# Kernel tuning notes

Measured on AMD Instinct MI355X. Metric: run time of the kernel, lower is better.

Reference implementation:

```python
import jax, jax.numpy as jnp
import numpy as np
from jax import lax

B, N, D, H, K = 8, 1024, 384, 6, 7
HD = D // H
EPS = 1e-5


def layer_norm(x, g, b):
    m = jnp.mean(x, axis=-1, keepdims=True)
    v = jnp.mean(jnp.square(x - m), axis=-1, keepdims=True)
    return (x - m) * lax.rsqrt(v + EPS) * g + b


def setup_inputs() -> dict:
    key = jax.random.key(0)
    ks = jax.random.split(key, 12)
    s = 0.02
    return {
        "x": jax.random.normal(ks[0], (B, N, D), jnp.float32),
        "qkv_w": jax.random.normal(ks[1], (3 * D, D), jnp.float32) * s,
        "qkv_b": jnp.zeros((3 * D,), jnp.float32),
        "proj_w": jax.random.normal(ks[2], (D, D), jnp.float32) * s,
        "proj_b": jnp.zeros((D,), jnp.float32),
        "t_before": jnp.eye(H, dtype=jnp.float32) + jax.random.normal(ks[3], (H, H), jnp.float32) * 0.01,
        "t_after": jnp.eye(H, dtype=jnp.float32) + jax.random.normal(ks[4], (H, H), jnp.float32) * 0.01,
        "dw_w": jax.random.normal(ks[5], (D, 1, K), jnp.float32) * s,
        "dw_b": jnp.zeros((D,), jnp.float32),
        "mlp_ln_g": jnp.ones((D,), jnp.float32),
        "mlp_ln_b": jnp.zeros((D,), jnp.float32),
        "norm1_g": jnp.ones((D,), jnp.float32),
        "norm1_b": jnp.zeros((D,), jnp.float32),
        "norm2_g": jnp.ones((D,), jnp.float32),
        "norm2_b": jnp.zeros((D,), jnp.float32),
        "fc1_w": jax.random.normal(ks[6], (4 * D, D), jnp.float32) * s,
        "fc1_b": jnp.zeros((4 * D,), jnp.float32),
        "fc2_w": jax.random.normal(ks[7], (D, 4 * D), jnp.float32) * s,
        "fc2_b": jnp.zeros((D,), jnp.float32),
    }


def reference(x, qkv_w, qkv_b, proj_w, proj_b, t_before, t_after, dw_w, dw_b,
              mlp_ln_g, mlp_ln_b, norm1_g, norm1_b, norm2_g, norm2_b,
              fc1_w, fc1_b, fc2_w, fc2_b):
    # ---- attention branch ----
    h = layer_norm(x, norm1_g, norm1_b)
    qkv = h @ qkv_w.T + qkv_b                                  # (B,N,3D)
    qkv = qkv.reshape(B, N, 3, H, HD).transpose(2, 0, 3, 1, 4)  # (3,B,H,N,hd)
    q, k, v = qkv[0], qkv[1], qkv[2]
    scale = HD ** -0.5
    scores = jnp.einsum('bhnd,bhmd->bhnm', q, k) * scale        # (B,H,N,N)
    scores = jnp.einsum('gh,bhnm->bgnm', t_before, scores)       # head-mix pre-softmax
    probs = jax.nn.softmax(scores, axis=-1)
    probs = jnp.einsum('gh,bhnm->bgnm', t_after, probs)          # head-mix post-softmax
    attn_out = jnp.einsum('bhnm,bhmd->bhnd', probs, v)           # (B,H,N,hd)
    attn_out = attn_out.transpose(0, 2, 1, 3).reshape(B, N, D)
    attn_out = attn_out @ proj_w.T + proj_b
    x = x + attn_out
    # ---- MLP branch ----
    h = layer_norm(x, norm2_g, norm2_b)
    # depthwise conv1d over tokens: (B,D,N), groups=D, same padding
    h_t = h.transpose(0, 2, 1)
    h_t = lax.conv_general_dilated(h_t, dw_w, window_strides=(1,),
                                   padding=[(K // 2, K // 2)],
                                   dimension_numbers=('NCH', 'OIH', 'NCH'),
                                   feature_group_count=D)
    h = h_t.transpose(0, 2, 1) + dw_b
    h = layer_norm(h, mlp_ln_g, mlp_ln_b)
    h = jax.nn.gelu(h @ fc1_w.T + fc1_b, approximate=False)
    h = h @ fc2_w.T + fc2_b
    return x + h
```

## Files before the change

### kernel.cpp

```cpp
#include <hip/hip_runtime.h>
#include <hip/hip_bf16.h>

#define BB 8
#define NN 1024
#define DD 384
#define HH 6
#define HD 64
#define BN 8192
#define D3 1152
#define D4 1536
#define SEC 3145728

typedef __attribute__((ext_vector_type(8))) short short8;
typedef __attribute__((ext_vector_type(4))) float f32x4;
typedef __attribute__((ext_vector_type(2))) float f32x2;

typedef __attribute__((address_space(3))) unsigned char as3_byte;
typedef __attribute__((address_space(1))) const unsigned char as1_byte;

__device__ __forceinline__ void gload16(const void* g, void* l){
  __builtin_amdgcn_global_load_lds((as1_byte*)g, (as3_byte*)l, 16, 0, 0);
}

__device__ __forceinline__ float b2f(unsigned short u){
  union{unsigned int i; float f;} x; x.i=((unsigned int)u)<<16; return x.f;
}
__device__ __forceinline__ unsigned short f2b(float f){
  unsigned int u=__float_as_uint(f);
  return (unsigned short)((u + 0x7FFFu + ((u>>16)&1u))>>16);
}

__global__ void cvt_kernel(const float* __restrict__ w0, const float* __restrict__ w1,
                           const float* __restrict__ w2, const float* __restrict__ w3,
                           unsigned short* __restrict__ out, float* __restrict__ lbuf){
  int i = blockIdx.x*256 + threadIdx.x;
  if (i < 442368)        out[i] = f2b(w0[i]);
  else if (i < 589824)   out[i] = f2b(w1[i - 442368]);
  else if (i < 1179648)  out[i] = f2b(w2[i - 589824]);
  else if (i < 1769472)  out[i] = f2b(w3[i - 1179648]);
  else if (i < 1818624)  lbuf[i - 1769472] = 0.f;
}

template<int OUTBF>
__global__ __launch_bounds__(128)
void ln_kernel(const float* __restrict__ in, const float* __restrict__ gg, const float* __restrict__ bb,
               float* __restrict__ outf, unsigned short* __restrict__ outb){
  int row = blockIdx.x, t = threadIdx.x;
  const float* r = in + (size_t)row*DD;
  float v0=r[t], v1=r[t+128], v2=r[t+256];
  float s=v0+v1+v2, q=v0*v0+v1*v1+v2*v2;
  #pragma unroll
  for (int o=32;o>0;o>>=1){ s+=__shfl_down(s,o); q+=__shfl_down(q,o); }
  __shared__ float ls[2], lq[2];
  if ((t&63)==0){ ls[t>>6]=s; lq[t>>6]=q; }
  __syncthreads();
  float S=ls[0]+ls[1], Q=lq[0]+lq[1];
  float mean=S*(1.0f/DD);
  float rstd=rsqrtf(Q*(1.0f/DD)-mean*mean+1e-5f);
  float o0=(v0-mean)*rstd*gg[t]+bb[t];
  float o1=(v1-mean)*rstd*gg[t+128]+bb[t+128];
  float o2=(v2-mean)*rstd*gg[t+256]+bb[t+256];
  if (OUTBF){ unsigned short* o=outb+(size_t)row*DD; o[t]=f2b(o0); o[t+128]=f2b(o1); o[t+256]=f2b(o2); }
  else      { float* o=outf+(size_t)row*DD; o[t]=o0; o[t+128]=o1; o[t+256]=o2; }
}

__global__ __launch_bounds__(128)
void conv_ln_kernel(const float* __restrict__ h2, const float* __restrict__ dww, const float* __restrict__ dwb,
                    const float* __restrict__ gg, const float* __restrict__ bb, unsigned short* __restrict__ out){
  int row=blockIdx.x, t=threadIdx.x;
  int bi=row>>10, n=row&1023;
  const float* base = h2 + (size_t)(bi<<10)*DD;
  float a[3];
  #pragma unroll
  for (int j=0;j<3;j++){
    int d=t+j*128;
    float acc=dwb[d];
    #pragma unroll
    for (int k=0;k<7;k++){
      int nn=n+k-3;
      if (nn>=0 && nn<NN) acc += dww[d*7+k]*base[(size_t)nn*DD + d];
    }
    a[j]=acc;
  }
  float s=a[0]+a[1]+a[2], q=a[0]*a[0]+a[1]*a[1]+a[2]*a[2];
  #pragma unroll
  for (int o=32;o>0;o>>=1){ s+=__shfl_down(s,o); q+=__shfl_down(q,o); }
  __shared__ float ls[2], lq[2];
  if ((t&63)==0){ ls[t>>6]=s; lq[t>>6]=q; }
  __syncthreads();
  float S=ls[0]+ls[1], Q=lq[0]+lq[1];
  float mean=S*(1.0f/DD);
  float rstd=rsqrtf(Q*(1.0f/DD)-mean*mean+1e-5f);
  unsigned short* o = out + (size_t)row*DD;
  #pragma unroll
  for (int j=0;j<3;j++){
    int d=t+j*128;
    o[d]=f2b((a[j]-mean)*rstd*gg[d]+bb[d]);
  }
}

template<int MODE, int TN>
__global__ __launch_bounds__(256)
void gemm_kernel(const unsigned short* __restrict__ A, const unsigned short* __restrict__ W,
                 const float* __restrict__ bias, const float* __restrict__ resid,
                 float* __restrict__ outf, unsigned short* __restrict__ outb,
                 unsigned char* __restrict__ v8out,
                 int Kdim, int Ncols){
  constexpr int JF = TN/32;
  __shared__ __align__(16) unsigned short lds_a[2][128*32];
  __shared__ __align__(16) unsigned short lds_b[2][TN*32];
  int t=threadIdx.x, lane=t&63, w=t>>6;
  int bm = blockIdx.x*128;
  int bn = blockIdx.y*TN;
  int wr = w>>1, wc = w&1;
  int rm = lane&15, r16 = lane>>4;
  f32x4 acc[4][JF] = {};
  char* ldsa_c = (char*)lds_a;
  char* ldsb_c = (char*)lds_b;
  int abyte[4], bbyte[JF];
  #pragma unroll
  for (int i=0;i<4;i++){
    int ra = wr*64 + i*16 + rm;
    abyte[i] = ra*64 + ((r16 ^ ((ra>>1)&3))*16);
  }
  #pragma unroll
  for (int j=0;j<JF;j++){
    int rb = wc*(TN/2) + j*16 + rm;
    bbyte[j] = rb*64 + ((r16 ^ ((rb>>1)&3))*16);
  }
  auto stage = [&](int buf, int k0){
    #pragma unroll
    for (int c=0;c<2;c++){
      int u = t + c*256;
      int row = u>>2, sl = (u&3) ^ ((row>>1)&3);
      gload16(A + (size_t)(bm+row)*Kdim + k0 + sl*8, ldsa_c + buf*8192 + u*16);
    }
    #pragma unroll
    for (int c=0;c<TN/64;c++){
      int u = t + c*256;
      int row = u>>2, sl = (u&3) ^ ((row>>1)&3);
      gload16(W + (size_t)(bn+row)*Kdim + k0 + sl*8, ldsb_c + buf*(TN*64) + u*16);
    }
  };
  int niter = Kdim>>5;
  stage(0, 0);
  __syncthreads();
  for (int it=0; it<niter; ++it){
    if (it+1<niter) stage((it+1)&1, (it+1)<<5);
    int ab = (it&1)*8192, bb2 = (it&1)*(TN*64);
    short8 af[4], bf[JF];
    #pragma unroll
    for (int i=0;i<4;i++) af[i]=*reinterpret_cast<const short8*>(ldsa_c + ab + abyte[i]);
    #pragma unroll
    for (int j=0;j<JF;j++) bf[j]=*reinterpret_cast<const short8*>(ldsb_c + bb2 + bbyte[j]);
    #pragma unroll
    for (int i=0;i<4;i++)
      #pragma unroll
      for (int j=0;j<JF;j++)
        acc[i][j]=__builtin_amdgcn_mfma_f32_16x16x32_bf16(af[i],bf[j],acc[i][j],0,0,0);
    __syncthreads();
  }
  #pragma unroll
  for (int i=0;i<4;i++){
    #pragma unroll
    for (int j=0;j<JF;j++){
      #pragma unroll
      for (int r=0;r<4;r++){
        int row = bm + wr*64 + i*16 + r16*4 + r;
        int col = bn + wc*(TN/2) + j*16 + rm;
        float v = acc[i][j][r] + bias[col];
        if (MODE==0){
          int c = col/384; int rem = col - c*384; int hh = rem>>6, d = rem&63;
          int bi = row>>10, nn = row&1023;
          if (c==2){
            int pk = __builtin_amdgcn_cvt_pk_fp8_f32(v, v, 0, false);
            v8out[(((size_t)(bi*6+hh))<<16) + ((size_t)d<<10) + nn] = (unsigned char)(pk & 0xff);
          } else {
            if (c==0) v *= 0.125f;
            outb[(size_t)c*SEC + (((size_t)(bi*6+hh))<<16) + (nn<<6) + d] = f2b(v);
          }
        } else if (MODE==1){
          size_t idx = (size_t)row*Ncols + col;
          outf[idx] = resid[idx] + v;
        } else {
          float ge = 0.5f*v*(1.0f+erff(v*0.70710678118654752f));
          outb[(size_t)row*Ncols + col] = f2b(ge);
        }
      }
    }
  }
}

__global__ __launch_bounds__(256, 2)
void smx_kernel(const unsigned short* __restrict__ qkv, const float* __restrict__ tbm,
                unsigned char* __restrict__ E, float* __restrict__ lbuf){
  __shared__ __align__(16) unsigned short Qs[6*16*64];
  __shared__ __align__(16) unsigned short Ks[6*64*64];
  __shared__ float lred[4][6][16];
  int t=threadIdx.x, lane=t&63, w=t>>6;
  int blk = blockIdx.x;
  int b = blk&7, nt = (blk>>3)&63, mh = blk>>9;
  int n0 = nt*16, mbase = mh<<9;
  int c16 = lane&15, r16 = lane>>4;
  const unsigned short* kbase = qkv + SEC + (((size_t)(b*6))<<16);
  #pragma unroll
  for (int i=0;i<3;i++){
    int u = t + i*256;
    int r = u>>3, s = (u&7) ^ (r&7);
    int h = r>>4, n = r&15;
    gload16(qkv + (((size_t)(b*6+h))<<16) + ((size_t)(n0+n)<<6) + s*8,
            (char*)Qs + u*16);
  }
  auto stageK = [&](int m0){
    #pragma unroll
    for (int i=0;i<12;i++){
      int u = t + i*256;
      int r = u>>3, s = (u&7) ^ (r&7);
      int h = r>>6, m = r&63;
      gload16(kbase + (((size_t)h)<<16) + ((size_t)(m0+m)<<6) + s*8,
              (char*)Ks + u*16);
    }
  };
  stageK(mbase);
  float tbr[36];
  #pragma unroll
  for (int i=0;i<36;i++) tbr[i]=tbm[i]*1.44269504088896f;
  __syncthreads();
  int sw = c16&7;
  short8 qf[6][2];
  #pragma unroll
  for (int h=0;h<6;h++){
    int qb = (h*16 + c16)*128;
    qf[h][0] = *(const short8*)((char*)Qs + qb + ((r16^sw)<<4));
    qf[h][1] = *(const short8*)((char*)Qs + qb + (((4+r16)^sw)<<4));
  }
  int kb0 = (w*16 + c16)*128 + ((r16^sw)<<4);
  int kb1 = (w*16 + c16)*128 + (((4+r16)^sw)<<4);
  float lsum[6] = {0.f,0.f,0.f,0.f,0.f,0.f};
  for (int mt=0; mt<8; ++mt){
    int m0 = mbase + mt*64;
    f32x4 aq[6] = {};
    __builtin_amdgcn_s_setprio(1);
    #pragma unroll
    for (int h=0;h<6;h++){
      short8 kf0 = *(const short8*)((char*)Ks + h*8192 + kb0);
      short8 kf1 = *(const short8*)((char*)Ks + h*8192 + kb1);
      aq[h] = __builtin_amdgcn_mfma_f32_16x16x32_bf16(kf0, qf[h][0], aq[h], 0,0,0);
      aq[h] = __builtin_amdgcn_mfma_f32_16x16x32_bf16(kf1, qf[h][1], aq[h], 0,0,0);
    }
    __builtin_amdgcn_s_setprio(0);
    __syncthreads();
    if (mt<7) stageK(m0+64);
    float ef[6][4];
    #pragma unroll
    for (int r=0;r<4;r++){
      float s0=aq[0][r], s1=aq[1][r], s2=aq[2][r],
            s3=aq[3][r], s4=aq[4][r], s5=aq[5][r];
      #pragma unroll
      for (int g=0;g<6;g++){
        float sm = tbr[g*6]*s0 + tbr[g*6+1]*s1 + tbr[g*6+2]*s2
                 + tbr[g*6+3]*s3 + tbr[g*6+4]*s4 + tbr[g*6+5]*s5;
        float e = __builtin_amdgcn_exp2f(sm);
        ef[g][r] = e;
        lsum[g] += e;
      }
    }
    #pragma unroll
    for (int g=0;g<6;g++){
      int pkv = __builtin_amdgcn_cvt_pk_fp8_f32(ef[g][0], ef[g][1], 0, false);
      pkv = __builtin_amdgcn_cvt_pk_fp8_f32(ef[g][2], ef[g][3], pkv, true);
      *(unsigned int*)(E + (((size_t)(b*6+g))<<20) + ((size_t)(n0+c16)<<10) + m0 + w*16 + r16*4)
        = (unsigned int)pkv;
    }
    if (mt<7) __syncthreads();
  }
  #pragma unroll
  for (int g=0;g<6;g++){
    lsum[g] += __shfl_xor(lsum[g],16);
    lsum[g] += __shfl_xor(lsum[g],32);
  }
  if (r16==0){
    #pragma unroll
    for (int g=0;g<6;g++) lred[w][g][c16] = lsum[g];
  }
  __syncthreads();
  if (w==0 && r16==0){
    #pragma unroll
    for (int g=0;g<6;g++){
      float l = lred[0][g][c16]+lred[1][g][c16]+lred[2][g][c16]+lred[3][g][c16];
      atomicAdd(&lbuf[(((size_t)(b*6+g))<<10) + n0 + c16], l);
    }
  }
}

__global__ __launch_bounds__(256, 2)
void pvmix_kernel(const unsigned char* __restrict__ E, const unsigned char* __restrict__ V8,
                  const float* __restrict__ lbuf, const float* __restrict__ tam,
                  unsigned short* __restrict__ outp){
  __shared__ __align__(16) unsigned char Es[6*16*64];
  __shared__ __align__(16) unsigned char Vs[6*64*64];
  __shared__ __align__(16) unsigned char pms[6*16*64];
  int t=threadIdx.x, lane=t&63, w=t>>6;
  int b = blockIdx.x&7, nt = blockIdx.x>>3;
  int n0 = nt*16;
  int c16 = lane&15, r16 = lane>>4;
  int mn = t&15, mg = (t>>4)&7, gh = t>>7;
  float cf[3][6];
  #pragma unroll
  for (int g=0;g<6;g++){
    float iv = 256.0f/lbuf[(((size_t)(b*6+g))<<10) + n0 + mn];
    #pragma unroll
    for (int j=0;j<3;j++) cf[j][g] = tam[(gh*3+j)*6 + g]*iv;
  }
  auto stageE = [&](int m0){
    #pragma unroll
    for (int i=0;i<2;i++){
      int u = t + i*256;
      if (u<384){
        int r = u>>2, s = (u&3) ^ (r&3);
        int g = r>>4, n = r&15;
        gload16(E + (((size_t)(b*6+g))<<20) + ((size_t)(n0+n)<<10) + m0 + s*16,
                (char*)Es + u*16);
      }
    }
  };
  auto stageV = [&](int m0){
    #pragma unroll
    for (int i=0;i<6;i++){
      int u = t + i*256;
      int r = u>>2, s = (u&3) ^ (r&3);
      int g = r>>6, d = r&63;
      gload16(V8 + (((size_t)(b*6+g))<<16) + ((size_t)d<<10) + m0 + s*16,
              (char*)Vs + u*16);
    }
  };
  stageE(0); stageV(0);
  __syncthreads();
  f32x4 acc[6] = {};
  for (int mt=0; mt<16; ++mt){
    float e[6][8];
    #pragma unroll
    for (int g=0;g<6;g++){
      int row = g*16 + mn;
      int byteo = row*64 + ((mg*8) ^ ((row&3)<<4));
      unsigned int lo = *(const unsigned int*)(Es + byteo);
      unsigned int hi = *(const unsigned int*)(Es + byteo + 4);
      f32x2 p0 = __builtin_amdgcn_cvt_pk_f32_fp8(lo, false);
      f32x2 p1 = __builtin_amdgcn_cvt_pk_f32_fp8(lo, true);
      f32x2 p2 = __builtin_amdgcn_cvt_pk_f32_fp8(hi, false);
      f32x2 p3 = __builtin_amdgcn_cvt_pk_f32_fp8(hi, true);
      e[g][0]=p0.x; e[g][1]=p0.y; e[g][2]=p1.x; e[g][3]=p1.y;
      e[g][4]=p2.x; e[g][5]=p2.y; e[g][6]=p3.x; e[g][7]=p3.y;
    }
    #pragma unroll
    for (int j=0;j<3;j++){
      float pm[8];
      #pragma unroll
      for (int m=0;m<8;m++)
        pm[m] = cf[j][0]*e[0][m]+cf[j][1]*e[1][m]+cf[j][2]*e[2][m]
              + cf[j][3]*e[3][m]+cf[j][4]*e[4][m]+cf[j][5]*e[5][m];
      int d0 = __builtin_amdgcn_cvt_pk_fp8_f32(pm[0], pm[1], 0, false);
      d0 = __builtin_amdgcn_cvt_pk_fp8_f32(pm[2], pm[3], d0, true);
      int d1 = __builtin_amdgcn_cvt_pk_fp8_f32(pm[4], pm[5], 0, false);
      d1 = __builtin_amdgcn_cvt_pk_fp8_f32(pm[6], pm[7], d1, true);
      int prow = (gh*3+j)*16 + mn;
      int pbyte = prow*64 + ((mg*8) ^ ((mn&7)<<3));
      *(unsigned int*)(pms + pbyte)     = (unsigned int)d0;
      *(unsigned int*)(pms + pbyte + 4) = (unsigned int)d1;
    }
    __syncthreads();
    if (mt<15) stageE((mt+1)*64);
    #pragma unroll
    for (int g=0;g<6;g++){
      int arow = g*16 + c16;
      int vrow = g*64 + w*16 + c16;
      #pragma unroll
      for (int kk=0;kk<2;kk++){
        long af = *(const long*)(pms + arow*64 + ((kk*32 + r16*8) ^ ((c16&7)<<3)));
        long bf = *(const long*)(Vs + vrow*64
                   + ((((kk*2 + (r16>>1)) ^ (vrow&3))<<4) + ((r16&1)<<3)));
        acc[g] = __builtin_amdgcn_mfma_f32_16x16x32_fp8_fp8(af, bf, acc[g], 0,0,0);
      }
    }
    __syncthreads();
    if (mt<15) stageV((mt+1)*64);
  }
  #pragma unroll
  for (int g=0;g<6;g++)
    #pragma unroll
    for (int r=0;r<4;r++){
      int n = n0 + r16*4 + r;
      int d = g*64 + w*16 + c16;
      outp[((size_t)(b*1024 + n))*DD + d] = f2b(acc[g][r] * 0.00390625f);
    }
}

extern "C" void kernel_launch(void* const* d_in, const int* in_sizes, int n_in,
                              void* d_out, int out_size, void* d_ws, size_t ws_size,
                              hipStream_t stream){
  const float* x      = (const float*)d_in[0];
  const float* qkv_w  = (const float*)d_in[1];
  const float* qkv_b  = (const float*)d_in[2];
  const float* proj_w = (const float*)d_in[3];
  const float* proj_b = (const float*)d_in[4];
  const float* t_before=(const float*)d_in[5];
  const float* t_after =(const float*)d_in[6];
  const float* dw_w   = (const float*)d_in[7];
  const float* dw_b   = (const float*)d_in[8];
  const float* mlp_g  = (const float*)d_in[9];
  const float* mlp_b  = (const float*)d_in[10];
  const float* n1_g   = (const float*)d_in[11];
  const float* n1_b   = (const float*)d_in[12];
  const float* n2_g   = (const float*)d_in[13];
  const float* n2_b   = (const float*)d_in[14];
  const float* fc1_w  = (const float*)d_in[15];
  const float* fc1_b  = (const float*)d_in[16];
  const float* fc2_w  = (const float*)d_in[17];
  const float* fc2_b  = (const float*)d_in[18];
  float* out = (float*)d_out;
  char* ws = (char*)d_ws;
  unsigned short* qkvwb = (unsigned short*)(ws + 0);
  unsigned short* projwb= (unsigned short*)(ws + 884736);
  unsigned short* fc1wb = (unsigned short*)(ws + 1179648);
  unsigned short* fc2wb = (unsigned short*)(ws + 2359296);
  unsigned short* hb    = (unsigned short*)(ws + 3538944);
  unsigned short* qkvb  = (unsigned short*)(ws + 9830400);
  unsigned char*  V8    = (unsigned char*) (ws + 28704768);
  float*          lbuf  = (float*)        (ws + 31850496);
  unsigned char*  Ebuf  = (unsigned char*) (ws + 34996224);
  unsigned short* attnb = (unsigned short*)(ws + 85327872);
  float*          x2    = (float*)(ws + 91619328);
  float* h2 = (float*)qkvb;
  unsigned short* hcln = hb;
  unsigned short* fc1o = (unsigned short*)Ebuf;

  cvt_kernel<<<7104,256,0,stream>>>(qkv_w, proj_w, fc1_w, fc2_w, qkvwb, lbuf);

  ln_kernel<1><<<BN,128,0,stream>>>(x, n1_g, n1_b, nullptr, hb);
  { dim3 g(BN/128, D3/128); gemm_kernel<0,128><<<g,256,0,stream>>>(hb, qkvwb, qkv_b, nullptr, nullptr, qkvb, V8, DD, D3); }
  smx_kernel<<<1024,256,0,stream>>>(qkvb, t_before, Ebuf, lbuf);
  pvmix_kernel<<<512,256,0,stream>>>(Ebuf, V8, lbuf, t_after, attnb);
  { dim3 g(BN/128, DD/64); gemm_kernel<1,64><<<g,256,0,stream>>>(attnb, projwb, proj_b, x, x2, nullptr, nullptr, DD, DD); }
  ln_kernel<0><<<BN,128,0,stream>>>(x2, n2_g, n2_b, h2, nullptr);
  conv_ln_kernel<<<BN,128,0,stream>>>(h2, dw_w, dw_b, mlp_g, mlp_b, hcln);
  { dim3 g(BN/128, D4/128); gemm_kernel<2,128><<<g,256,0,stream>>>(hcln, fc1wb, fc1_b, nullptr, nullptr, fc1o, nullptr, DD, D4); }
  { dim3 g(BN/128, DD/64); gemm_kernel<1,64><<<g,256,0,stream>>>(fc1o, fc2wb, fc2_b, x2, out, nullptr, nullptr, D4, DD); }
}
```

Before: 208.0 us.

## Store Q/K as FP8 and use FP8 MFMA with 32-row query tiles in softmax

The QKV GEMM now writes Q and K as FP8 bytes instead of bf16, and folds the attention scale into the head-mix coefficients rather than scaling Q. The scores kernel loads these FP8 tiles with an adjusted swizzle and uses fp8 MFMA instructions. Each block now handles 32 query rows, which halves the grid and doubles the reuse of every staged K tile. The aim is to halve Q/K memory traffic and LDS footprint and to raise MFMA throughput, at the cost of lower precision in the attention scores.

```diff
diff --git a/kernel.cpp b/kernel.cpp
--- a/kernel.cpp
+++ b/kernel.cpp
@@ -104,7 +104,7 @@
 void gemm_kernel(const unsigned short* __restrict__ A, const unsigned short* __restrict__ W,
                  const float* __restrict__ bias, const float* __restrict__ resid,
                  float* __restrict__ outf, unsigned short* __restrict__ outb,
-                 unsigned char* __restrict__ v8out,
+                 unsigned char* __restrict__ qk8out, unsigned char* __restrict__ v8out,
                  int Kdim, int Ncols){
   constexpr int JF = TN/32;
   __shared__ __align__(16) unsigned short lds_a[2][128*32];
@@ -172,12 +172,11 @@
         if (MODE==0){
           int c = col/384; int rem = col - c*384; int hh = rem>>6, d = rem&63;
           int bi = row>>10, nn = row&1023;
+          unsigned char pk = (unsigned char)(__builtin_amdgcn_cvt_pk_fp8_f32(v, v, 0, false) & 0xff);
           if (c==2){
-            int pk = __builtin_amdgcn_cvt_pk_fp8_f32(v, v, 0, false);
-            v8out[(((size_t)(bi*6+hh))<<16) + ((size_t)d<<10) + nn] = (unsigned char)(pk & 0xff);
+            v8out[(((size_t)(bi*6+hh))<<16) + ((size_t)d<<10) + nn] = pk;
           } else {
-            if (c==0) v *= 0.125f;
-            outb[(size_t)c*SEC + (((size_t)(bi*6+hh))<<16) + (nn<<6) + d] = f2b(v);
+            qk8out[(size_t)c*SEC + (((size_t)(bi*6+hh))<<16) + ((size_t)nn<<6) + d] = pk;
           }
         } else if (MODE==1){
           size_t idx = (size_t)row*Ncols + col;
@@ -191,105 +190,108 @@
   }
 }
 
-__global__ __launch_bounds__(256, 2)
-void smx_kernel(const unsigned short* __restrict__ qkv, const float* __restrict__ tbm,
+__global__ __launch_bounds__(256, 4)
+void smx_kernel(const unsigned char* __restrict__ qk8, const float* __restrict__ tbm,
                 unsigned char* __restrict__ E, float* __restrict__ lbuf){
-  __shared__ __align__(16) unsigned short Qs[6*16*64];
-  __shared__ __align__(16) unsigned short Ks[6*64*64];
-  __shared__ float lred[4][6][16];
+  __shared__ __align__(16) unsigned char Qs[6*32*64];
+  __shared__ __align__(16) unsigned char Ks[6*64*64];
+  __shared__ float lred[4][6][32];
   int t=threadIdx.x, lane=t&63, w=t>>6;
   int blk = blockIdx.x;
-  int b = blk&7, nt = (blk>>3)&63, mh = blk>>9;
-  int n0 = nt*16, mbase = mh<<9;
+  int b = blk&7, nt = (blk>>3)&31, mh = blk>>8;
+  int n0 = nt*32, mbase = mh<<9;
   int c16 = lane&15, r16 = lane>>4;
-  const unsigned short* kbase = qkv + SEC + (((size_t)(b*6))<<16);
+  int mq = w*16;
+  const unsigned char* q8 = qk8;
+  const unsigned char* k8 = qk8 + SEC;
   #pragma unroll
   for (int i=0;i<3;i++){
     int u = t + i*256;
-    int r = u>>3, s = (u&7) ^ (r&7);
-    int h = r>>4, n = r&15;
-    gload16(qkv + (((size_t)(b*6+h))<<16) + ((size_t)(n0+n)<<6) + s*8,
-            (char*)Qs + u*16);
+    int r = u>>2, s = (u&3) ^ (r&3);
+    int h = r>>5, n = r&31;
+    gload16(q8 + (((size_t)(b*6+h))<<16) + ((size_t)(n0+n)<<6) + s*16, (char*)Qs + u*16);
   }
   auto stageK = [&](int m0){
     #pragma unroll
-    for (int i=0;i<12;i++){
+    for (int i=0;i<6;i++){
       int u = t + i*256;
-      int r = u>>3, s = (u&7) ^ (r&7);
+      int r = u>>2, s = (u&3) ^ (r&3);
       int h = r>>6, m = r&63;
-      gload16(kbase + (((size_t)h)<<16) + ((size_t)(m0+m)<<6) + s*8,
-              (char*)Ks + u*16);
+      gload16(k8 + (((size_t)(b*6+h))<<16) + ((size_t)(m0+m)<<6) + s*16, (char*)Ks + u*16);
     }
   };
   stageK(mbase);
   float tbr[36];
   #pragma unroll
-  for (int i=0;i<36;i++) tbr[i]=tbm[i]*1.44269504088896f;
-  __syncthreads();
-  int sw = c16&7;
-  short8 qf[6][2];
-  #pragma unroll
-  for (int h=0;h<6;h++){
-    int qb = (h*16 + c16)*128;
-    qf[h][0] = *(const short8*)((char*)Qs + qb + ((r16^sw)<<4));
-    qf[h][1] = *(const short8*)((char*)Qs + qb + (((4+r16)^sw)<<4));
-  }
-  int kb0 = (w*16 + c16)*128 + ((r16^sw)<<4);
-  int kb1 = (w*16 + c16)*128 + (((4+r16)^sw)<<4);
-  float lsum[6] = {0.f,0.f,0.f,0.f,0.f,0.f};
+  for (int i=0;i<36;i++) tbr[i] = tbm[i]*0.125f*1.44269504088896f;
+  __syncthreads();
+  float lsum[6][2] = {};
   for (int mt=0; mt<8; ++mt){
     int m0 = mbase + mt*64;
-    f32x4 aq[6] = {};
+    f32x4 aq[6][2] = {};
     __builtin_amdgcn_s_setprio(1);
     #pragma unroll
     for (int h=0;h<6;h++){
-      short8 kf0 = *(const short8*)((char*)Ks + h*8192 + kb0);
-      short8 kf1 = *(const short8*)((char*)Ks + h*8192 + kb1);
-      aq[h] = __builtin_amdgcn_mfma_f32_16x16x32_bf16(kf0, qf[h][0], aq[h], 0,0,0);
-      aq[h] = __builtin_amdgcn_mfma_f32_16x16x32_bf16(kf1, qf[h][1], aq[h], 0,0,0);
+      int krow = h*64 + mq + c16;
+      #pragma unroll
+      for (int kk=0;kk<2;kk++){
+        long kf = *(const long*)(Ks + krow*64 + (((kk*2+(r16>>1)) ^ (krow&3))<<4) + ((r16&1)<<3));
+        #pragma unroll
+        for (int ih=0;ih<2;ih++){
+          int qrow = h*32 + ih*16 + c16;
+          long qf = *(const long*)(Qs + qrow*64 + (((kk*2+(r16>>1)) ^ (qrow&3))<<4) + ((r16&1)<<3));
+          aq[h][ih] = __builtin_amdgcn_mfma_f32_16x16x32_fp8_fp8(kf, qf, aq[h][ih], 0,0,0);
+        }
+      }
     }
     __builtin_amdgcn_s_setprio(0);
     __syncthreads();
     if (mt<7) stageK(m0+64);
-    float ef[6][4];
-    #pragma unroll
-    for (int r=0;r<4;r++){
-      float s0=aq[0][r], s1=aq[1][r], s2=aq[2][r],
-            s3=aq[3][r], s4=aq[4][r], s5=aq[5][r];
+    #pragma unroll
+    for (int ih=0;ih<2;ih++){
+      float ef[6][4];
+      #pragma unroll
+      for (int r=0;r<4;r++){
+        float s0=aq[0][ih][r], s1=aq[1][ih][r], s2=aq[2][ih][r],
+              s3=aq[3][ih][r], s4=aq[4][ih][r], s5=aq[5][ih][r];
+        #pragma unroll
+        for (int g=0;g<6;g++){
+          float sm = tbr[g*6]*s0 + tbr[g*6+1]*s1 + tbr[g*6+2]*s2
+                   + tbr[g*6+3]*s3 + tbr[g*6+4]*s4 + tbr[g*6+5]*s5;
+          float e = __builtin_amdgcn_exp2f(sm);
+          ef[g][r] = e;
+          lsum[g][ih] += e;
+        }
+      }
       #pragma unroll
       for (int g=0;g<6;g++){
-        float sm = tbr[g*6]*s0 + tbr[g*6+1]*s1 + tbr[g*6+2]*s2
-                 + tbr[g*6+3]*s3 + tbr[g*6+4]*s4 + tbr[g*6+5]*s5;
-        float e = __builtin_amdgcn_exp2f(sm);
-        ef[g][r] = e;
-        lsum[g] += e;
-      }
-    }
+        int pkv = __builtin_amdgcn_cvt_pk_fp8_f32(ef[g][0], ef[g][1], 0, false);
+        pkv = __builtin_amdgcn_cvt_pk_fp8_f32(ef[g][2], ef[g][3], pkv, true);
+        *(unsigned int*)(E + (((size_t)(b*6+g))<<20) + ((size_t)(n0+ih*16+c16)<<10) + m0 + mq + r16*4)
+          = (unsigned int)pkv;
+      }
+    }
+    if (mt<7) __syncthreads();
+  }
+  #pragma unroll
+  for (int g=0;g<6;g++)
+    #pragma unroll
+    for (int ih=0;ih<2;ih++){
+      lsum[g][ih] += __shfl_xor(lsum[g][ih],16);
+      lsum[g][ih] += __shfl_xor(lsum[g][ih],32);
+    }
+  if (r16==0){
     #pragma unroll
     for (int g=0;g<6;g++){
-      int pkv = __builtin_amdgcn_cvt_pk_fp8_f32(ef[g][0], ef[g][1], 0, false);
-      pkv = __builtin_amdgcn_cvt_pk_fp8_f32(ef[g][2], ef[g][3], pkv, true);
-      *(unsigned int*)(E + (((size_t)(b*6+g))<<20) + ((size_t)(n0+c16)<<10) + m0 + w*16 + r16*4)
-        = (unsigned int)pkv;
-    }
-    if (mt<7) __syncthreads();
-  }
-  #pragma unroll
-  for (int g=0;g<6;g++){
-    lsum[g] += __shfl_xor(lsum[g],16);
-    lsum[g] += __shfl_xor(lsum[g],32);
-  }
-  if (r16==0){
-    #pragma unroll
-    for (int g=0;g<6;g++) lred[w][g][c16] = lsum[g];
-  }
-  __syncthreads();
-  if (w==0 && r16==0){
-    #pragma unroll
-    for (int g=0;g<6;g++){
-      float l = lred[0][g][c16]+lred[1][g][c16]+lred[2][g][c16]+lred[3][g][c16];
-      atomicAdd(&lbuf[(((size_t)(b*6+g))<<10) + n0 + c16], l);
-    }
+      lred[w][g][c16]    = lsum[g][0];
+      lred[w][g][16+c16] = lsum[g][1];
+    }
+  }
+  __syncthreads();
+  if (t<192){
+    int g = t>>5, n32 = t&31;
+    float l = lred[0][g][n32]+lred[1][g][n32]+lred[2][g][n32]+lred[3][g][n32];
+    atomicAdd(&lbuf[(((size_t)(b*6+g))<<10) + n0 + n32], l);
   }
 }
 
@@ -424,25 +426,25 @@
   unsigned short* fc1wb = (unsigned short*)(ws + 1179648);
   unsigned short* fc2wb = (unsigned short*)(ws + 2359296);
   unsigned short* hb    = (unsigned short*)(ws + 3538944);
-  unsigned short* qkvb  = (unsigned short*)(ws + 9830400);
+  unsigned char*  qk8   = (unsigned char*) (ws + 9830400);
   unsigned char*  V8    = (unsigned char*) (ws + 28704768);
   float*          lbuf  = (float*)        (ws + 31850496);
   unsigned char*  Ebuf  = (unsigned char*) (ws + 34996224);
   unsigned short* attnb = (unsigned short*)(ws + 85327872);
   float*          x2    = (float*)(ws + 91619328);
-  float* h2 = (float*)qkvb;
+  float* h2 = (float*)qk8;
   unsigned short* hcln = hb;
   unsigned short* fc1o = (unsigned short*)Ebuf;
 
   cvt_kernel<<<7104,256,0,stream>>>(qkv_w, proj_w, fc1_w, fc2_w, qkvwb, lbuf);
 
   ln_kernel<1><<<BN,128,0,stream>>>(x, n1_g, n1_b, nullptr, hb);
-  { dim3 g(BN/128, D3/128); gemm_kernel<0,128><<<g,256,0,stream>>>(hb, qkvwb, qkv_b, nullptr, nullptr, qkvb, V8, DD, D3); }
-  smx_kernel<<<1024,256,0,stream>>>(qkvb, t_before, Ebuf, lbuf);
+  { dim3 g(BN/128, D3/128); gemm_kernel<0,128><<<g,256,0,stream>>>(hb, qkvwb, qkv_b, nullptr, nullptr, nullptr, qk8, V8, DD, D3); }
+  smx_kernel<<<512,256,0,stream>>>(qk8, t_before, Ebuf, lbuf);
   pvmix_kernel<<<512,256,0,stream>>>(Ebuf, V8, lbuf, t_after, attnb);
-  { dim3 g(BN/128, DD/64); gemm_kernel<1,64><<<g,256,0,stream>>>(attnb, projwb, proj_b, x, x2, nullptr, nullptr, DD, DD); }
+  { dim3 g(BN/128, DD/64); gemm_kernel<1,64><<<g,256,0,stream>>>(attnb, projwb, proj_b, x, x2, nullptr, nullptr, nullptr, DD, DD); }
   ln_kernel<0><<<BN,128,0,stream>>>(x2, n2_g, n2_b, h2, nullptr);
   conv_ln_kernel<<<BN,128,0,stream>>>(h2, dw_w, dw_b, mlp_g, mlp_b, hcln);
-  { dim3 g(BN/128, D4/128); gemm_kernel<2,128><<<g,256,0,stream>>>(hcln, fc1wb, fc1_b, nullptr, nullptr, fc1o, nullptr, DD, D4); }
-  { dim3 g(BN/128, DD/64); gemm_kernel<1,64><<<g,256,0,stream>>>(fc1o, fc2wb, fc2_b, x2, out, nullptr, nullptr, D4, DD); }
-}
+  { dim3 g(BN/128, D4/128); gemm_kernel<2,128><<<g,256,0,stream>>>(hcln, fc1wb, fc1_b, nullptr, nullptr, fc1o, nullptr, nullptr, DD, D4); }
+  { dim3 g(BN/128, DD/64); gemm_kernel<1,64><<<g,256,0,stream>>>(fc1o, fc2wb, fc2_b, x2, out, nullptr, nullptr, nullptr, D4, DD); }
+}
```

Measured after the change: 241.8 us. +16.2%, slower.

## Store Q/K as fp8 in MFMA fragment layout and drop LDS staging in softmax

Applied to the files above, without the earlier changes.

The QKV GEMM now writes Q and K as fp8 in a pre-swizzled fragment layout, so the softmax kernel loads MFMA operands straight from global memory and uses fp8 MFMA instead of staging bf16 tiles through LDS with barriers. The 1/8 scale moves into the head-mix matrix. The row-sum atomics are replaced with per-half partial sums that pvmix adds together, which also removes the zeroing in the conversion kernel. Occupancy hint raised to 4. Risk: lower Q/K precision in the scores and uncoalesced byte-wide scattered stores from the GEMM epilogue.

```diff
diff --git a/kernel.cpp b/kernel.cpp
--- a/kernel.cpp
+++ b/kernel.cpp
@@ -14,6 +14,7 @@
 typedef __attribute__((ext_vector_type(8))) short short8;
 typedef __attribute__((ext_vector_type(4))) float f32x4;
 typedef __attribute__((ext_vector_type(2))) float f32x2;
+typedef long v2i64 __attribute__((ext_vector_type(2)));
 
 typedef __attribute__((address_space(3))) unsigned char as3_byte;
 typedef __attribute__((address_space(1))) const unsigned char as1_byte;
@@ -32,13 +33,12 @@
 
 __global__ void cvt_kernel(const float* __restrict__ w0, const float* __restrict__ w1,
                            const float* __restrict__ w2, const float* __restrict__ w3,
-                           unsigned short* __restrict__ out, float* __restrict__ lbuf){
+                           unsigned short* __restrict__ out){
   int i = blockIdx.x*256 + threadIdx.x;
   if (i < 442368)        out[i] = f2b(w0[i]);
   else if (i < 589824)   out[i] = f2b(w1[i - 442368]);
   else if (i < 1179648)  out[i] = f2b(w2[i - 589824]);
   else if (i < 1769472)  out[i] = f2b(w3[i - 1179648]);
-  else if (i < 1818624)  lbuf[i - 1769472] = 0.f;
 }
 
 template<int OUTBF>
@@ -104,7 +104,7 @@
 void gemm_kernel(const unsigned short* __restrict__ A, const unsigned short* __restrict__ W,
                  const float* __restrict__ bias, const float* __restrict__ resid,
                  float* __restrict__ outf, unsigned short* __restrict__ outb,
-                 unsigned char* __restrict__ v8out,
+                 unsigned char* __restrict__ qk8out, unsigned char* __restrict__ v8out,
                  int Kdim, int Ncols){
   constexpr int JF = TN/32;
   __shared__ __align__(16) unsigned short lds_a[2][128*32];
@@ -172,12 +172,14 @@
         if (MODE==0){
           int c = col/384; int rem = col - c*384; int hh = rem>>6, d = rem&63;
           int bi = row>>10, nn = row&1023;
+          unsigned char pk = (unsigned char)(__builtin_amdgcn_cvt_pk_fp8_f32(v, v, 0, false) & 0xff);
           if (c==2){
-            int pk = __builtin_amdgcn_cvt_pk_fp8_f32(v, v, 0, false);
-            v8out[(((size_t)(bi*6+hh))<<16) + ((size_t)d<<10) + nn] = (unsigned char)(pk & 0xff);
+            v8out[(((size_t)(bi*6+hh))<<16) + ((size_t)d<<10) + nn] = pk;
           } else {
-            if (c==0) v *= 0.125f;
-            outb[(size_t)c*SEC + (((size_t)(bi*6+hh))<<16) + (nn<<6) + d] = f2b(v);
+            size_t fa = ((size_t)c*SEC)
+                      + ((((size_t)(bi*6+hh))<<6) + (nn>>4))*1024
+                      + ((((d>>3)&3)*16 + (nn&15))<<4) + ((d>>5)*8) + (d&7);
+            qk8out[fa] = pk;
           }
         } else if (MODE==1){
           size_t idx = (size_t)row*Ncols + col;
@@ -191,66 +193,37 @@
   }
 }
 
-__global__ __launch_bounds__(256, 2)
-void smx_kernel(const unsigned short* __restrict__ qkv, const float* __restrict__ tbm,
-                unsigned char* __restrict__ E, float* __restrict__ lbuf){
-  __shared__ __align__(16) unsigned short Qs[6*16*64];
-  __shared__ __align__(16) unsigned short Ks[6*64*64];
+__global__ __launch_bounds__(256, 4)
+void smx_kernel(const unsigned char* __restrict__ qk8, const float* __restrict__ tbm,
+                unsigned char* __restrict__ E, float* __restrict__ lpart){
   __shared__ float lred[4][6][16];
   int t=threadIdx.x, lane=t&63, w=t>>6;
-  int blk = blockIdx.x;
+  int blk=blockIdx.x;
   int b = blk&7, nt = (blk>>3)&63, mh = blk>>9;
-  int n0 = nt*16, mbase = mh<<9;
-  int c16 = lane&15, r16 = lane>>4;
-  const unsigned short* kbase = qkv + SEC + (((size_t)(b*6))<<16);
-  #pragma unroll
-  for (int i=0;i<3;i++){
-    int u = t + i*256;
-    int r = u>>3, s = (u&7) ^ (r&7);
-    int h = r>>4, n = r&15;
-    gload16(qkv + (((size_t)(b*6+h))<<16) + ((size_t)(n0+n)<<6) + s*8,
-            (char*)Qs + u*16);
-  }
-  auto stageK = [&](int m0){
-    #pragma unroll
-    for (int i=0;i<12;i++){
-      int u = t + i*256;
-      int r = u>>3, s = (u&7) ^ (r&7);
-      int h = r>>6, m = r&63;
-      gload16(kbase + (((size_t)h)<<16) + ((size_t)(m0+m)<<6) + s*8,
-              (char*)Ks + u*16);
-    }
-  };
-  stageK(mbase);
+  int n0 = nt*16, mbase = mh*512;
+  int c16=lane&15, r16=lane>>4;
+  const unsigned char* q8f = qk8;
+  const unsigned char* k8f = qk8 + SEC;
+  v2i64 qf[6];
+  #pragma unroll
+  for (int h=0;h<6;h++)
+    qf[h] = *(const v2i64*)(q8f + (((((size_t)(b*6+h))<<6) + (n0>>4))<<10) + lane*16);
   float tbr[36];
   #pragma unroll
-  for (int i=0;i<36;i++) tbr[i]=tbm[i]*1.44269504088896f;
-  __syncthreads();
-  int sw = c16&7;
-  short8 qf[6][2];
-  #pragma unroll
-  for (int h=0;h<6;h++){
-    int qb = (h*16 + c16)*128;
-    qf[h][0] = *(const short8*)((char*)Qs + qb + ((r16^sw)<<4));
-    qf[h][1] = *(const short8*)((char*)Qs + qb + (((4+r16)^sw)<<4));
-  }
-  int kb0 = (w*16 + c16)*128 + ((r16^sw)<<4);
-  int kb1 = (w*16 + c16)*128 + (((4+r16)^sw)<<4);
-  float lsum[6] = {0.f,0.f,0.f,0.f,0.f,0.f};
+  for (int i=0;i<36;i++) tbr[i] = tbm[i]*0.125f*1.44269504088896f;
+  float lsum[6]={0.f,0.f,0.f,0.f,0.f,0.f};
   for (int mt=0; mt<8; ++mt){
-    int m0 = mbase + mt*64;
+    int m0 = mbase + mt*64 + w*16;
+    v2i64 kf[6];
+    #pragma unroll
+    for (int h=0;h<6;h++)
+      kf[h] = *(const v2i64*)(k8f + (((((size_t)(b*6+h))<<6) + (m0>>4))<<10) + lane*16);
     f32x4 aq[6] = {};
-    __builtin_amdgcn_s_setprio(1);
     #pragma unroll
     for (int h=0;h<6;h++){
-      short8 kf0 = *(const short8*)((char*)Ks + h*8192 + kb0);
-      short8 kf1 = *(const short8*)((char*)Ks + h*8192 + kb1);
-      aq[h] = __builtin_amdgcn_mfma_f32_16x16x32_bf16(kf0, qf[h][0], aq[h], 0,0,0);
-      aq[h] = __builtin_amdgcn_mfma_f32_16x16x32_bf16(kf1, qf[h][1], aq[h], 0,0,0);
-    }
-    __builtin_amdgcn_s_setprio(0);
-    __syncthreads();
-    if (mt<7) stageK(m0+64);
+      aq[h] = __builtin_amdgcn_mfma_f32_16x16x32_fp8_fp8(kf[h][0], qf[h][0], aq[h], 0,0,0);
+      aq[h] = __builtin_amdgcn_mfma_f32_16x16x32_fp8_fp8(kf[h][1], qf[h][1], aq[h], 0,0,0);
+    }
     float ef[6][4];
     #pragma unroll
     for (int r=0;r<4;r++){
@@ -269,10 +242,9 @@
     for (int g=0;g<6;g++){
       int pkv = __builtin_amdgcn_cvt_pk_fp8_f32(ef[g][0], ef[g][1], 0, false);
       pkv = __builtin_amdgcn_cvt_pk_fp8_f32(ef[g][2], ef[g][3], pkv, true);
-      *(unsigned int*)(E + (((size_t)(b*6+g))<<20) + ((size_t)(n0+c16)<<10) + m0 + w*16 + r16*4)
+      *(unsigned int*)(E + (((size_t)(b*6+g))<<20) + ((size_t)(n0+c16)<<10) + m0 + r16*4)
         = (unsigned int)pkv;
     }
-    if (mt<7) __syncthreads();
   }
   #pragma unroll
   for (int g=0;g<6;g++){
@@ -288,14 +260,14 @@
     #pragma unroll
     for (int g=0;g<6;g++){
       float l = lred[0][g][c16]+lred[1][g][c16]+lred[2][g][c16]+lred[3][g][c16];
-      atomicAdd(&lbuf[(((size_t)(b*6+g))<<10) + n0 + c16], l);
+      lpart[(((size_t)(mh*48 + b*6+g))<<10) + n0 + c16] = l;
     }
   }
 }
 
 __global__ __launch_bounds__(256, 2)
 void pvmix_kernel(const unsigned char* __restrict__ E, const unsigned char* __restrict__ V8,
-                  const float* __restrict__ lbuf, const float* __restrict__ tam,
+                  const float* __restrict__ lpart, const float* __restrict__ tam,
                   unsigned short* __restrict__ outp){
   __shared__ __align__(16) unsigned char Es[6*16*64];
   __shared__ __align__(16) unsigned char Vs[6*64*64];
@@ -308,7 +280,9 @@
   float cf[3][6];
   #pragma unroll
   for (int g=0;g<6;g++){
-    float iv = 256.0f/lbuf[(((size_t)(b*6+g))<<10) + n0 + mn];
+    float l0 = lpart[(((size_t)(b*6+g))<<10) + n0 + mn];
+    float l1 = lpart[(((size_t)(48 + b*6+g))<<10) + n0 + mn];
+    float iv = 256.0f/(l0 + l1);
     #pragma unroll
     for (int j=0;j<3;j++) cf[j][g] = tam[(gh*3+j)*6 + g]*iv;
   }
@@ -424,25 +398,25 @@
   unsigned short* fc1wb = (unsigned short*)(ws + 1179648);
   unsigned short* fc2wb = (unsigned short*)(ws + 2359296);
   unsigned short* hb    = (unsigned short*)(ws + 3538944);
-  unsigned short* qkvb  = (unsigned short*)(ws + 9830400);
+  unsigned char*  qk8   = (unsigned char*) (ws + 9830400);
   unsigned char*  V8    = (unsigned char*) (ws + 28704768);
-  float*          lbuf  = (float*)        (ws + 31850496);
+  float*          lpart = (float*)        (ws + 31850496);
   unsigned char*  Ebuf  = (unsigned char*) (ws + 34996224);
   unsigned short* attnb = (unsigned short*)(ws + 85327872);
   float*          x2    = (float*)(ws + 91619328);
-  float* h2 = (float*)qkvb;
+  float* h2 = (float*)qk8;
   unsigned short* hcln = hb;
   unsigned short* fc1o = (unsigned short*)Ebuf;
 
-  cvt_kernel<<<7104,256,0,stream>>>(qkv_w, proj_w, fc1_w, fc2_w, qkvwb, lbuf);
+  cvt_kernel<<<6912,256,0,stream>>>(qkv_w, proj_w, fc1_w, fc2_w, qkvwb);
 
   ln_kernel<1><<<BN,128,0,stream>>>(x, n1_g, n1_b, nullptr, hb);
-  { dim3 g(BN/128, D3/128); gemm_kernel<0,128><<<g,256,0,stream>>>(hb, qkvwb, qkv_b, nullptr, nullptr, qkvb, V8, DD, D3); }
-  smx_kernel<<<1024,256,0,stream>>>(qkvb, t_before, Ebuf, lbuf);
-  pvmix_kernel<<<512,256,0,stream>>>(Ebuf, V8, lbuf, t_after, attnb);
-  { dim3 g(BN/128, DD/64); gemm_kernel<1,64><<<g,256,0,stream>>>(attnb, projwb, proj_b, x, x2, nullptr, nullptr, DD, DD); }
+  { dim3 g(BN/128, D3/128); gemm_kernel<0,128><<<g,256,0,stream>>>(hb, qkvwb, qkv_b, nullptr, nullptr, nullptr, qk8, V8, DD, D3); }
+  smx_kernel<<<1024,256,0,stream>>>(qk8, t_before, Ebuf, lpart);
+  pvmix_kernel<<<512,256,0,stream>>>(Ebuf, V8, lpart, t_after, attnb);
+  { dim3 g(BN/128, DD/64); gemm_kernel<1,64><<<g,256,0,stream>>>(attnb, projwb, proj_b, x, x2, nullptr, nullptr, nullptr, DD, DD); }
   ln_kernel<0><<<BN,128,0,stream>>>(x2, n2_g, n2_b, h2, nullptr);
   conv_ln_kernel<<<BN,128,0,stream>>>(h2, dw_w, dw_b, mlp_g, mlp_b, hcln);
-  { dim3 g(BN/128, D4/128); gemm_kernel<2,128><<<g,256,0,stream>>>(hcln, fc1wb, fc1_b, nullptr, nullptr, fc1o, nullptr, DD, D4); }
-  { dim3 g(BN/128, DD/64); gemm_kernel<1,64><<<g,256,0,stream>>>(fc1o, fc2wb, fc2_b, x2, out, nullptr, nullptr, D4, DD); }
-}
+  { dim3 g(BN/128, D4/128); gemm_kernel<2,128><<<g,256,0,stream>>>(hcln, fc1wb, fc1_b, nullptr, nullptr, fc1o, nullptr, nullptr, DD, D4); }
+  { dim3 g(BN/128, DD/64); gemm_kernel<1,64><<<g,256,0,stream>>>(fc1o, fc2wb, fc2_b, x2, out, nullptr, nullptr, nullptr, D4, DD); }
+}
```

Measured after the change: 195.2 us. -6.2%, faster.
